# Optimization experiments

Hardware: AMD Instinct MI355X
Metric: run time of the kernel (lower is better)

Reference implementation:

```python
import jax, jax.numpy as jnp
import numpy as np

NUM_HEADS = 4
NUM_GROUPS = 8
EPS = 1e-5


def group_norm(x, gamma, beta):
    # x: [b, c, h, w], GroupNorm with NUM_GROUPS groups, eps=1e-5
    b, c, h, w = x.shape
    xg = x.reshape(b, NUM_GROUPS, (c // NUM_GROUPS) * h * w)
    mean = jnp.mean(xg, axis=-1, keepdims=True)
    var = jnp.var(xg, axis=-1, keepdims=True)
    xn = ((xg - mean) * jax.lax.rsqrt(var + EPS)).reshape(b, c, h, w)
    return xn * gamma[None, :, None, None] + beta[None, :, None, None]


def setup_inputs() -> dict:
    key = jax.random.key(0)
    ks = jax.random.split(key, 4)
    b, c, h, w = 4, 256, 64, 64
    x = jax.random.normal(ks[0], (b, c, h, w), dtype=jnp.float32)
    gamma = jnp.ones((c,), dtype=jnp.float32)
    beta = jnp.zeros((c,), dtype=jnp.float32)
    w_qkv = jax.random.normal(ks[1], (3 * c, c), dtype=jnp.float32) * (c ** -0.5)
    b_qkv = jnp.zeros((3 * c,), dtype=jnp.float32)
    w_proj = jax.random.normal(ks[2], (c, c), dtype=jnp.float32) * (c ** -0.5)
    b_proj = jnp.zeros((c,), dtype=jnp.float32)
    return {"x": x, "gamma": gamma, "beta": beta, "w_qkv": w_qkv,
            "b_qkv": b_qkv, "w_proj": w_proj, "b_proj": b_proj}


def reference(x, gamma, beta, w_qkv, b_qkv, w_proj, b_proj):
    b, c, h, w = x.shape
    heads = NUM_HEADS
    dim = c // heads
    n = h * w
    residual = x
    xn = group_norm(x, gamma, beta)
    # 1x1 conv == per-pixel linear: [b,c,h,w] x [3c,c] -> [b,3c,h,w]
    qkv = jnp.einsum('bchw,oc->bohw', xn, w_qkv) + b_qkv[None, :, None, None]
    # channel layout: (three, heads, dim)
    qkv = qkv.reshape(b, 3, heads, dim, n)            # [b,3,H,D,N]
    qkv = jnp.transpose(qkv, (1, 0, 2, 4, 3))         # [3,b,H,N,D]
    q, k, v = qkv[0], qkv[1], qkv[2]
    scale = dim ** -0.5
    scores = jnp.einsum('bhid,bhjd->bhij', q * scale, k)  # [b,H,N,N]
    attn = jax.nn.softmax(scores, axis=-1)
    out = jnp.einsum('bhij,bhjd->bhid', attn, v)          # [b,H,N,D]
    out = jnp.transpose(out, (0, 1, 3, 2)).reshape(b, c, h, w)
    out = jnp.einsum('bchw,oc->bohw', out, w_proj) + b_proj[None, :, None, None]
    return out + residual
```

## Files before the change

### kernel.cpp

```cpp
#include <hip/hip_runtime.h>
#include <stdint.h>

typedef unsigned short ushort_t;
typedef __attribute__((ext_vector_type(8))) short bf16x8;
typedef __attribute__((ext_vector_type(4))) float f32x4;
typedef __attribute__((ext_vector_type(16))) float f32x16;
typedef __attribute__((ext_vector_type(4))) unsigned int u32x4;

__device__ __forceinline__ ushort_t f2bf(float f) {
  union { float f; unsigned u; } v; v.f = f;
  unsigned r = v.u + 0x7fffu + ((v.u >> 16) & 1u);
  return (ushort_t)(r >> 16);
}
__device__ __forceinline__ unsigned bfbits(float f) {
  union { float f; unsigned u; } v; v.f = f; return v.u;
}
__device__ __forceinline__ unsigned pack_trunc(float lo, float hi) {
#if __has_builtin(__builtin_amdgcn_perm)
  return __builtin_amdgcn_perm(bfbits(hi), bfbits(lo), 0x07060302u);
#else
  return (bfbits(lo) >> 16) | (bfbits(hi) & 0xffff0000u);
#endif
}
__device__ __forceinline__ unsigned pack_rn(float lo, float hi) {
  return (unsigned)f2bf(lo) | ((unsigned)f2bf(hi) << 16);
}
__device__ __forceinline__ void swap32(unsigned &a, unsigned &b) {
#if __has_builtin(__builtin_amdgcn_permlane32_swap)
  auto r = __builtin_amdgcn_permlane32_swap(a, b, false, false);
  a = r[0]; b = r[1];
#else
  asm volatile("v_permlane32_swap_b32 %0, %1" : "+v"(a), "+v"(b));
#endif
}

#define SCALE_Q 0.18033688011112042f
#define EXP_BIAS 23.083109273961734f

__global__ __launch_bounds__(256)
void gn_stats1(const float* __restrict__ x, float2* __restrict__ partial) {
  int blk = blockIdx.x, tid = threadIdx.x;
  const float* base = x + (size_t)blk * 16384;
  float s = 0.f, ss = 0.f;
  for (int i = tid * 4; i < 16384; i += 1024) {
    float4 v = *(const float4*)(base + i);
    s  += v.x + v.y + v.z + v.w;
    ss += v.x*v.x + v.y*v.y + v.z*v.z + v.w*v.w;
  }
  __shared__ float rs[256], rss[256];
  rs[tid] = s; rss[tid] = ss;
  __syncthreads();
  for (int off = 128; off > 0; off >>= 1) {
    if (tid < off) { rs[tid] += rs[tid+off]; rss[tid] += rss[tid+off]; }
    __syncthreads();
  }
  if (tid == 0) partial[blk] = make_float2(rs[0], rss[0]);
}

__global__ __launch_bounds__(64)
void gn_stats2(const float2* __restrict__ partial, float* __restrict__ stats) {
  int g = threadIdx.x;
  if (g < 32) {
    float s = 0.f, ss = 0.f;
    #pragma unroll
    for (int k = 0; k < 8; k++) { float2 p = partial[g*8 + k]; s += p.x; ss += p.y; }
    float mean = s * (1.f/131072.f);
    float var  = ss * (1.f/131072.f) - mean*mean;
    stats[g*2]   = mean;
    stats[g*2+1] = rsqrtf(var + 1e-5f);
  }
}

__global__ __launch_bounds__(256)
void gn_apply_t(const float* __restrict__ x, const float* __restrict__ stats,
                const float* __restrict__ gamma, const float* __restrict__ beta,
                ushort_t* __restrict__ xn_t, int b0) {
  int blk = blockIdx.x;
  int tid = threadIdx.x;
  int ct = blk & 7;
  int nt = (blk >> 3) & 15;
  int bl = blk >> 7;
  int b  = b0 + bl;
  int c0 = ct * 32;
  float mean = stats[(b*8 + ct)*2];
  float rstd = stats[(b*8 + ct)*2 + 1];
  __shared__ ushort_t Ls[32][264];
  for (int idx = tid; idx < 32*64; idx += 256) {
    int cc = idx >> 6, seg = idx & 63;
    float ga = gamma[c0+cc], be = beta[c0+cc];
    float a = rstd * ga;
    float bb = be - mean * a;
    float4 v = *(const float4*)(x + ((size_t)(b*256 + c0 + cc))*4096 + nt*256 + seg*4);
    ushort4 t4 = make_ushort4(f2bf(v.x*a+bb), f2bf(v.y*a+bb), f2bf(v.z*a+bb), f2bf(v.w*a+bb));
    *(ushort4*)&Ls[cc][seg*4] = t4;
  }
  __syncthreads();
  for (int idx = tid; idx < 256*4; idx += 256) {
    int n = idx >> 2, seg = idx & 3;
    union { ushort_t u[8]; uint4 v; } pk;
    #pragma unroll
    for (int e = 0; e < 8; e++) pk.u[e] = Ls[seg*8 + e][n];
    *(uint4*)(xn_t + ((size_t)(bl*4096 + nt*256 + n))*256 + c0 + seg*8) = pk.v;
  }
}

__global__ __launch_bounds__(256)
void wconv2(const float* __restrict__ wq, const float* __restrict__ wp,
            ushort_t* __restrict__ oq, ushort_t* __restrict__ op) {
  int blk = blockIdx.x;
  const float* w; ushort_t* o; int i;
  if (blk < 192) { w = wq; o = oq; i = blk*256 + threadIdx.x; }
  else           { w = wp; o = op; i = (blk-192)*256 + threadIdx.x; }
  float4 v = *(const float4*)(w + (size_t)i*4);
  *(ushort4*)(o + (size_t)i*4) = make_ushort4(f2bf(v.x), f2bf(v.y), f2bf(v.z), f2bf(v.w));
}

__global__ __launch_bounds__(256)
void gemm_qkv(const ushort_t* __restrict__ A, const ushort_t* __restrict__ Bt,
              const float* __restrict__ bias, ushort_t* __restrict__ q,
              ushort_t* __restrict__ kbuf, ushort_t* __restrict__ vt, int b0) {
  int blk = blockIdx.x;
  int nt = blk % 12, mt = blk / 12;
  int m0 = mt*128, n0 = nt*64;
  int tid = threadIdx.x;
  int wave = tid >> 6, lane = tid & 63, quad = lane >> 4, l16 = lane & 15;
  __shared__ ushort_t As[128][40];
  __shared__ ushort_t Bs[64][40];
  __shared__ ushort_t Lt[64][136];
  f32x4 acc[2][4];
  #pragma unroll
  for (int i = 0; i < 2; i++)
    #pragma unroll
    for (int j = 0; j < 4; j++) acc[i][j] = (f32x4){0.f,0.f,0.f,0.f};

  for (int k0 = 0; k0 < 256; k0 += 32) {
    #pragma unroll
    for (int i = tid; i < 512; i += 256) {
      int row = i >> 2, seg = i & 3;
      *(uint4*)&As[row][seg*8] = *(const uint4*)(A + (size_t)(m0+row)*256 + k0 + seg*8);
    }
    {
      int row = tid >> 2, seg = tid & 3;
      *(uint4*)&Bs[row][seg*8] = *(const uint4*)(Bt + (size_t)(n0+row)*256 + k0 + seg*8);
    }
    __syncthreads();
    bf16x8 af[2], bfr[4];
    #pragma unroll
    for (int t = 0; t < 2; t++) af[t]  = *(const bf16x8*)&As[wave*32 + t*16 + l16][quad*8];
    #pragma unroll
    for (int t = 0; t < 4; t++) bfr[t] = *(const bf16x8*)&Bs[t*16 + l16][quad*8];
    #pragma unroll
    for (int ti = 0; ti < 2; ti++)
      #pragma unroll
      for (int jn = 0; jn < 4; jn++)
        acc[ti][jn] = __builtin_amdgcn_mfma_f32_16x16x32_bf16(af[ti], bfr[jn], acc[ti][jn], 0, 0, 0);
    __syncthreads();
  }

  int region = nt >> 2;
  if (region == 0) {
    #pragma unroll
    for (int jn = 0; jn < 4; jn++) {
      int n = n0 + jn*16 + l16;
      float bv = bias[n];
      #pragma unroll
      for (int ti = 0; ti < 2; ti++) {
        int mrow = m0 + wave*32 + ti*16 + quad*4;
        #pragma unroll
        for (int r = 0; r < 4; r++)
          q[(size_t)(b0*4096 + mrow + r)*256 + n] = f2bf((acc[ti][jn][r] + bv) * SCALE_Q);
      }
    }
  } else if (region == 1) {
    #pragma unroll
    for (int jn = 0; jn < 4; jn++) {
      int n = n0 + jn*16 + l16;
      float bv = bias[n];
      #pragma unroll
      for (int ti = 0; ti < 2; ti++) {
        int mrow = m0 + wave*32 + ti*16 + quad*4;
        #pragma unroll
        for (int r = 0; r < 4; r++)
          kbuf[(size_t)(b0*4096 + mrow + r)*256 + (n - 256)] = f2bf(acc[ti][jn][r] + bv);
      }
    }
  } else {
    int hh = nt - 8;
    int b_loc = m0 >> 12;
    #pragma unroll
    for (int jn = 0; jn < 4; jn++) {
      int n = n0 + jn*16 + l16;
      float bv = bias[n];
      int drow = jn*16 + l16;
      #pragma unroll
      for (int ti = 0; ti < 2; ti++) {
        int tcol = wave*32 + ti*16 + quad*4;
        uint2 w;
        w.x = pack_rn(acc[ti][jn][0] + bv, acc[ti][jn][1] + bv);
        w.y = pack_rn(acc[ti][jn][2] + bv, acc[ti][jn][3] + bv);
        *(uint2*)&Lt[drow][tcol] = w;
      }
    }
    __syncthreads();
    size_t vb_ = ((size_t)((b0 + b_loc)*4 + hh)*64)*4096 + (size_t)(m0 & 4095);
    for (int idx = tid; idx < 1024; idx += 256) {
      int dd = idx >> 4, toff = (idx & 15)*8;
      *(uint4*)(vt + vb_ + (size_t)dd*4096 + toff) = *(const uint4*)&Lt[dd][toff];
    }
  }
}

__global__ __launch_bounds__(256, 2)
void attn(ushort_t* __restrict__ q, const ushort_t* __restrict__ k,
          const ushort_t* __restrict__ vt) {
  int blk = blockIdx.x;
  int it = blk & 31;
  int h  = (blk >> 5) & 3;
  int b  = blk >> 7;
  int i0 = it * 128;
  int tid = threadIdx.x;
  int wave = tid >> 6, lane = tid & 63;
  int q32 = lane & 31, hi = lane >> 5;

  __shared__ ushort_t Ks[2][64][72];
  __shared__ ushort_t Vs[2][64][72];

  const ushort_t* kbase = k + (size_t)(b*4096)*256 + h*64;
  const ushort_t* vbase = vt + (size_t)(b*4 + h)*64*4096;
  ushort_t* qrow = q + (size_t)(b*4096 + i0 + wave*32 + q32)*256 + h*64;

  bf16x8 qb0 = *(const bf16x8*)(qrow      + hi*8);
  bf16x8 qb1 = *(const bf16x8*)(qrow + 16 + hi*8);
  bf16x8 qb2 = *(const bf16x8*)(qrow + 32 + hi*8);
  bf16x8 qb3 = *(const bf16x8*)(qrow + 48 + hi*8);

  bf16x8 ones;
  #pragma unroll
  for (int e = 0; e < 8; e++) ones[e] = (short)0x3F80;

  f32x16 bias_init;
  #pragma unroll
  for (int r = 0; r < 16; r++) bias_init[r] = -EXP_BIAS;

  f32x16 o_acc0, o_acc1, l_acc;
  #pragma unroll
  for (int r = 0; r < 16; r++) { o_acc0[r] = 0.f; o_acc1[r] = 0.f; l_acc[r] = 0.f; }

  int sr = tid >> 2, sc = (tid & 3) * 16;
  uint4 rk0, rk1, rv0, rv1;
  #define LOADK(JT) { int j0n = (JT)*64; \
    rk0 = *(const uint4*)(kbase + (size_t)(j0n + sr)*256 + sc); \
    rk1 = *(const uint4*)(kbase + (size_t)(j0n + sr)*256 + sc + 8); }
  #define WRITEK(BI) { \
    *(uint4*)&Ks[BI][sr][sc]     = rk0; \
    *(uint4*)&Ks[BI][sr][sc + 8] = rk1; }
  #define LOADV(JT) { int j0n = (JT)*64; \
    rv0 = *(const uint4*)(vbase + (size_t)sr*4096 + j0n + sc); \
    rv1 = *(const uint4*)(vbase + (size_t)sr*4096 + j0n + sc + 8); }
  #define WRITEV(BI) { \
    *(uint4*)&Vs[BI][sr][sc]     = rv0; \
    *(uint4*)&Vs[BI][sr][sc + 8] = rv1; }

  #define COMPUTE_SUB32(BI, JB) { \
    bf16x8 kb0 = *(const bf16x8*)&Ks[BI][(JB) + q32][hi*8]; \
    bf16x8 kb1 = *(const bf16x8*)&Ks[BI][(JB) + q32][16 + hi*8]; \
    bf16x8 kb2 = *(const bf16x8*)&Ks[BI][(JB) + q32][32 + hi*8]; \
    bf16x8 kb3 = *(const bf16x8*)&Ks[BI][(JB) + q32][48 + hi*8]; \
    __builtin_amdgcn_s_setprio(1); \
    f32x16 s_ = __builtin_amdgcn_mfma_f32_32x32x16_bf16(kb0, qb0, bias_init, 0, 0, 0); \
    s_ = __builtin_amdgcn_mfma_f32_32x32x16_bf16(kb1, qb1, s_, 0, 0, 0); \
    s_ = __builtin_amdgcn_mfma_f32_32x32x16_bf16(kb2, qb2, s_, 0, 0, 0); \
    s_ = __builtin_amdgcn_mfma_f32_32x32x16_bf16(kb3, qb3, s_, 0, 0, 0); \
    _Pragma("unroll") \
    for (int r = 0; r < 16; r++) s_[r] = __builtin_exp2f(s_[r]); \
    unsigned pkA = pack_trunc(s_[0],  s_[1]),  pkB = pack_trunc(s_[2],  s_[3]); \
    unsigned pkC = pack_trunc(s_[4],  s_[5]),  pkD = pack_trunc(s_[6],  s_[7]); \
    unsigned pkE = pack_trunc(s_[8],  s_[9]),  pkF = pack_trunc(s_[10], s_[11]); \
    unsigned pkG = pack_trunc(s_[12], s_[13]), pkH = pack_trunc(s_[14], s_[15]); \
    swap32(pkA, pkC); swap32(pkB, pkD);    \
    swap32(pkE, pkG); swap32(pkF, pkH);    \
    u32x4 w0_ = {pkA, pkB, pkC, pkD}; \
    u32x4 w1_ = {pkE, pkF, pkG, pkH}; \
    bf16x8 pb0 = __builtin_bit_cast(bf16x8, w0_); \
    bf16x8 pb1 = __builtin_bit_cast(bf16x8, w1_); \
    bf16x8 vb00 = *(const bf16x8*)&Vs[BI][q32     ][(JB) + hi*8]; \
    bf16x8 vb01 = *(const bf16x8*)&Vs[BI][q32     ][(JB) + 16 + hi*8]; \
    bf16x8 vb10 = *(const bf16x8*)&Vs[BI][32 + q32][(JB) + hi*8]; \
    bf16x8 vb11 = *(const bf16x8*)&Vs[BI][32 + q32][(JB) + 16 + hi*8]; \
    o_acc0 = __builtin_amdgcn_mfma_f32_32x32x16_bf16(vb00, pb0, o_acc0, 0, 0, 0); \
    o_acc0 = __builtin_amdgcn_mfma_f32_32x32x16_bf16(vb01, pb1, o_acc0, 0, 0, 0); \
    o_acc1 = __builtin_amdgcn_mfma_f32_32x32x16_bf16(vb10, pb0, o_acc1, 0, 0, 0); \
    o_acc1 = __builtin_amdgcn_mfma_f32_32x32x16_bf16(vb11, pb1, o_acc1, 0, 0, 0); \
    l_acc  = __builtin_amdgcn_mfma_f32_32x32x16_bf16(ones, pb0, l_acc, 0, 0, 0); \
    l_acc  = __builtin_amdgcn_mfma_f32_32x32x16_bf16(ones, pb1, l_acc, 0, 0, 0); \
    __builtin_amdgcn_s_setprio(0); \
  }

  LOADK(0); LOADV(0); WRITEK(0); WRITEV(0);
  __syncthreads();

  for (int jt = 0; jt < 64; jt++) {
    int cur = jt & 1;
    if (jt < 63) LOADK(jt + 1);
    COMPUTE_SUB32(cur, 0)
    if (jt < 63) { WRITEK(cur ^ 1); LOADV(jt + 1); }
    COMPUTE_SUB32(cur, 32)
    if (jt < 63) WRITEV(cur ^ 1);
    __syncthreads();
  }
  #undef LOADK
  #undef LOADV
  #undef WRITEK
  #undef WRITEV
  #undef COMPUTE_SUB32

  float inv = 1.f / l_acc[0];

  #pragma unroll
  for (int g = 0; g < 4; g++) {
    ushort4 u;
    u.x = f2bf(o_acc0[g*4+0]*inv); u.y = f2bf(o_acc0[g*4+1]*inv);
    u.z = f2bf(o_acc0[g*4+2]*inv); u.w = f2bf(o_acc0[g*4+3]*inv);
    *(ushort4*)(qrow + g*8 + hi*4) = u;
  }
  #pragma unroll
  for (int g = 0; g < 4; g++) {
    ushort4 u;
    u.x = f2bf(o_acc1[g*4+0]*inv); u.y = f2bf(o_acc1[g*4+1]*inv);
    u.z = f2bf(o_acc1[g*4+2]*inv); u.w = f2bf(o_acc1[g*4+3]*inv);
    *(ushort4*)(qrow + 32 + g*8 + hi*4) = u;
  }
}

__global__ __launch_bounds__(256)
void gemm_proj(const ushort_t* __restrict__ A,
               const ushort_t* __restrict__ Bt,
               const float* __restrict__ bias, const float* __restrict__ resid,
               float* __restrict__ out, int col_base) {
  int blk = blockIdx.x;
  int mt = blk & 1, nt = blk >> 1;
  int m0 = mt*128, n0 = nt*64;
  int tid = threadIdx.x;
  int wave = tid >> 6, lane = tid & 63, quad = lane >> 4, l16 = lane & 15;
  __shared__ ushort_t As[128][40];
  __shared__ ushort_t Bs[64][40];
  f32x4 acc[2][4];
  #pragma unroll
  for (int i = 0; i < 2; i++)
    #pragma unroll
    for (int j = 0; j < 4; j++) acc[i][j] = (f32x4){0.f,0.f,0.f,0.f};

  for (int k0 = 0; k0 < 256; k0 += 32) {
    #pragma unroll
    for (int i = tid; i < 512; i += 256) {
      int row = i >> 2, seg = i & 3;
      *(uint4*)&As[row][seg*8] = *(const uint4*)(A + (size_t)(m0+row)*256 + k0 + seg*8);
    }
    {
      int row = tid >> 2, seg = tid & 3;
      *(uint4*)&Bs[row][seg*8] = *(const uint4*)(Bt + (size_t)(n0+row)*256 + k0 + seg*8);
    }
    __syncthreads();
    bf16x8 af[2], bfr[4];
    #pragma unroll
    for (int t = 0; t < 2; t++) af[t]  = *(const bf16x8*)&As[wave*32 + t*16 + l16][quad*8];
    #pragma unroll
    for (int t = 0; t < 4; t++) bfr[t] = *(const bf16x8*)&Bs[t*16 + l16][quad*8];
    #pragma unroll
    for (int ti = 0; ti < 2; ti++)
      #pragma unroll
      for (int jn = 0; jn < 4; jn++)
        acc[ti][jn] = __builtin_amdgcn_mfma_f32_16x16x32_bf16(af[ti], bfr[jn], acc[ti][jn], 0, 0, 0);
    __syncthreads();
  }
  #pragma unroll
  for (int jn = 0; jn < 4; jn++) {
    int col = col_base + n0 + jn*16 + l16;
    int bb = col >> 12;
    int np = col & 4095;
    #pragma unroll
    for (int ti = 0; ti < 2; ti++) {
      int o = m0 + wave*32 + ti*16 + quad*4;
      #pragma unroll
      for (int r = 0; r < 4; r++) {
        int oo = o + r;
        size_t addr = ((size_t)(bb*256 + oo))*4096 + np;
        out[addr] = acc[ti][jn][r] + bias[oo] + resid[addr];
      }
    }
  }
}

extern "C" void kernel_launch(void* const* d_in, const int* in_sizes, int n_in,
                              void* d_out, int out_size, void* d_ws, size_t ws_size,
                              hipStream_t stream) {
  const float* x      = (const float*)d_in[0];
  const float* gamma  = (const float*)d_in[1];
  const float* beta   = (const float*)d_in[2];
  const float* w_qkv  = (const float*)d_in[3];
  const float* b_qkv  = (const float*)d_in[4];
  const float* w_proj = (const float*)d_in[5];
  const float* b_proj = (const float*)d_in[6];
  float* out = (float*)d_out;

  char* ws = (char*)d_ws;
  float*  stats    = (float*)ws;
  float2* partial  = (float2*)(ws + 1024);
  ushort_t* wqkv_bf  = (ushort_t*)(ws + 4096);
  ushort_t* wproj_bf = (ushort_t*)(ws + 397312);
  char* big = ws + 528384;

  gn_stats1<<<dim3(256), dim3(256), 0, stream>>>(x, partial);
  gn_stats2<<<dim3(1), dim3(64), 0, stream>>>(partial, stats);
  wconv2<<<dim3(256), dim3(256), 0, stream>>>(w_qkv, w_proj, wqkv_bf, wproj_bf);

  if (ws_size >= (size_t)528384 + 3*(size_t)8388608 + (size_t)4194304) {
    ushort_t* q    = (ushort_t*)big;
    ushort_t* kbuf = (ushort_t*)(big + (size_t)8388608);
    ushort_t* vt   = (ushort_t*)(big + (size_t)16777216);
    ushort_t* xn   = (ushort_t*)(big + (size_t)25165824);
    for (int c = 0; c < 2; c++) {
      int b0 = c * 2;
      gn_apply_t<<<dim3(256), dim3(256), 0, stream>>>(x, stats, gamma, beta, xn, b0);
      gemm_qkv<<<dim3(768), dim3(256), 0, stream>>>(xn, wqkv_bf, b_qkv, q, kbuf, vt, b0);
    }
    attn<<<dim3(512), dim3(256), 0, stream>>>(q, kbuf, vt);
    gemm_proj<<<dim3(512), dim3(256), 0, stream>>>(wproj_bf, q, b_proj, x, out, 0);
  } else {
    ushort_t* q_c  = (ushort_t*)big;
    ushort_t* k_c  = (ushort_t*)(big + (size_t)2097152);
    ushort_t* vt_c = (ushort_t*)(big + (size_t)4194304);
    ushort_t* xn_c = (ushort_t*)(big + (size_t)6291456);
    for (int b0 = 0; b0 < 4; b0++) {
      gn_apply_t<<<dim3(128), dim3(256), 0, stream>>>(x, stats, gamma, beta, xn_c, b0);
      gemm_qkv<<<dim3(384), dim3(256), 0, stream>>>(xn_c, wqkv_bf, b_qkv, q_c, k_c, vt_c, 0);
      attn<<<dim3(128), dim3(256), 0, stream>>>(q_c, k_c, vt_c);
      gemm_proj<<<dim3(128), dim3(256), 0, stream>>>(wproj_bf, q_c, b_proj, x, out, b0*4096);
    }
  }
}
```

Before: 246.9 us.

## Split attention KV sequence across wave pairs and merge partial outputs in LDS

The attention kernel now gives each block 64 query rows instead of 128. Its four waves form two pairs, and each pair handles half of the key/value sequence (split-K). Partial output and row-sum accumulators are combined through shared memory at the end, and the grid doubles to 1024 blocks. This is meant to raise the number of blocks and improve occupancy and load balance across CUs. The cost is that each block's K/V tiles are reused by fewer query rows, so L2 traffic for K/V rises, and there is an extra LDS reduction and barrier. Summing the partials without rescaling is valid because the exp uses a fixed bias rather than a running max.

```diff
diff --git a/kernel.cpp b/kernel.cpp
--- a/kernel.cpp
+++ b/kernel.cpp
@@ -214,20 +214,22 @@
 void attn(ushort_t* __restrict__ q, const ushort_t* __restrict__ k,
           const ushort_t* __restrict__ vt) {
   int blk = blockIdx.x;
-  int it = blk & 31;
-  int h  = (blk >> 5) & 3;
-  int b  = blk >> 7;
-  int i0 = it * 128;
+  int it = blk & 63;
+  int h  = (blk >> 6) & 3;
+  int b  = blk >> 8;
+  int i0 = it * 64;
   int tid = threadIdx.x;
   int wave = tid >> 6, lane = tid & 63;
   int q32 = lane & 31, hi = lane >> 5;
-
-  __shared__ ushort_t Ks[2][64][72];
-  __shared__ ushort_t Vs[2][64][72];
-
-  const ushort_t* kbase = k + (size_t)(b*4096)*256 + h*64;
-  const ushort_t* vbase = vt + (size_t)(b*4 + h)*64*4096;
-  ushort_t* qrow = q + (size_t)(b*4096 + i0 + wave*32 + q32)*256 + h*64;
+  int ks = wave >> 1;
+  int qw = wave & 1;
+
+  __shared__ ushort_t Ks[2][2][32][68];
+  __shared__ ushort_t Vs[2][2][64][44];
+
+  const ushort_t* kbase = k + (size_t)(b*4096 + ks*2048)*256 + h*64;
+  const ushort_t* vbase = vt + (size_t)(b*4 + h)*64*4096 + ks*2048;
+  ushort_t* qrow = q + (size_t)(b*4096 + i0 + qw*32 + q32)*256 + h*64;
 
   bf16x8 qb0 = *(const bf16x8*)(qrow      + hi*8);
   bf16x8 qb1 = *(const bf16x8*)(qrow + 16 + hi*8);
@@ -246,26 +248,28 @@
   #pragma unroll
   for (int r = 0; r < 16; r++) { o_acc0[r] = 0.f; o_acc1[r] = 0.f; l_acc[r] = 0.f; }
 
-  int sr = tid >> 2, sc = (tid & 3) * 16;
+  int t = tid & 127, st = tid >> 7;
+  int sr = t >> 2, sc = (t & 3) * 16;
+  int vr = t >> 1, vc = (t & 1) * 16;
   uint4 rk0, rk1, rv0, rv1;
-  #define LOADK(JT) { int j0n = (JT)*64; \
-    rk0 = *(const uint4*)(kbase + (size_t)(j0n + sr)*256 + sc); \
-    rk1 = *(const uint4*)(kbase + (size_t)(j0n + sr)*256 + sc + 8); }
+  #define LOADK(JT) { \
+    rk0 = *(const uint4*)(kbase + (size_t)((JT)*32 + sr)*256 + sc); \
+    rk1 = *(const uint4*)(kbase + (size_t)((JT)*32 + sr)*256 + sc + 8); }
   #define WRITEK(BI) { \
-    *(uint4*)&Ks[BI][sr][sc]     = rk0; \
-    *(uint4*)&Ks[BI][sr][sc + 8] = rk1; }
-  #define LOADV(JT) { int j0n = (JT)*64; \
-    rv0 = *(const uint4*)(vbase + (size_t)sr*4096 + j0n + sc); \
-    rv1 = *(const uint4*)(vbase + (size_t)sr*4096 + j0n + sc + 8); }
+    *(uint4*)&Ks[st][BI][sr][sc]     = rk0; \
+    *(uint4*)&Ks[st][BI][sr][sc + 8] = rk1; }
+  #define LOADV(JT) { \
+    rv0 = *(const uint4*)(vbase + (size_t)vr*4096 + (JT)*32 + vc); \
+    rv1 = *(const uint4*)(vbase + (size_t)vr*4096 + (JT)*32 + vc + 8); }
   #define WRITEV(BI) { \
-    *(uint4*)&Vs[BI][sr][sc]     = rv0; \
-    *(uint4*)&Vs[BI][sr][sc + 8] = rv1; }
-
-  #define COMPUTE_SUB32(BI, JB) { \
-    bf16x8 kb0 = *(const bf16x8*)&Ks[BI][(JB) + q32][hi*8]; \
-    bf16x8 kb1 = *(const bf16x8*)&Ks[BI][(JB) + q32][16 + hi*8]; \
-    bf16x8 kb2 = *(const bf16x8*)&Ks[BI][(JB) + q32][32 + hi*8]; \
-    bf16x8 kb3 = *(const bf16x8*)&Ks[BI][(JB) + q32][48 + hi*8]; \
+    *(uint4*)&Vs[st][BI][vr][vc]     = rv0; \
+    *(uint4*)&Vs[st][BI][vr][vc + 8] = rv1; }
+
+  #define COMPUTE_SUB32(BI) { \
+    bf16x8 kb0 = *(const bf16x8*)&Ks[st][BI][q32][hi*8]; \
+    bf16x8 kb1 = *(const bf16x8*)&Ks[st][BI][q32][16 + hi*8]; \
+    bf16x8 kb2 = *(const bf16x8*)&Ks[st][BI][q32][32 + hi*8]; \
+    bf16x8 kb3 = *(const bf16x8*)&Ks[st][BI][q32][48 + hi*8]; \
     __builtin_amdgcn_s_setprio(1); \
     f32x16 s_ = __builtin_amdgcn_mfma_f32_32x32x16_bf16(kb0, qb0, bias_init, 0, 0, 0); \
     s_ = __builtin_amdgcn_mfma_f32_32x32x16_bf16(kb1, qb1, s_, 0, 0, 0); \
@@ -283,10 +287,10 @@
     u32x4 w1_ = {pkE, pkF, pkG, pkH}; \
     bf16x8 pb0 = __builtin_bit_cast(bf16x8, w0_); \
     bf16x8 pb1 = __builtin_bit_cast(bf16x8, w1_); \
-    bf16x8 vb00 = *(const bf16x8*)&Vs[BI][q32     ][(JB) + hi*8]; \
-    bf16x8 vb01 = *(const bf16x8*)&Vs[BI][q32     ][(JB) + 16 + hi*8]; \
-    bf16x8 vb10 = *(const bf16x8*)&Vs[BI][32 + q32][(JB) + hi*8]; \
-    bf16x8 vb11 = *(const bf16x8*)&Vs[BI][32 + q32][(JB) + 16 + hi*8]; \
+    bf16x8 vb00 = *(const bf16x8*)&Vs[st][BI][q32     ][hi*8]; \
+    bf16x8 vb01 = *(const bf16x8*)&Vs[st][BI][q32     ][16 + hi*8]; \
+    bf16x8 vb10 = *(const bf16x8*)&Vs[st][BI][32 + q32][hi*8]; \
+    bf16x8 vb11 = *(const bf16x8*)&Vs[st][BI][32 + q32][16 + hi*8]; \
     o_acc0 = __builtin_amdgcn_mfma_f32_32x32x16_bf16(vb00, pb0, o_acc0, 0, 0, 0); \
     o_acc0 = __builtin_amdgcn_mfma_f32_32x32x16_bf16(vb01, pb1, o_acc0, 0, 0, 0); \
     o_acc1 = __builtin_amdgcn_mfma_f32_32x32x16_bf16(vb10, pb0, o_acc1, 0, 0, 0); \
@@ -301,11 +305,9 @@
 
   for (int jt = 0; jt < 64; jt++) {
     int cur = jt & 1;
-    if (jt < 63) LOADK(jt + 1);
-    COMPUTE_SUB32(cur, 0)
-    if (jt < 63) { WRITEK(cur ^ 1); LOADV(jt + 1); }
-    COMPUTE_SUB32(cur, 32)
-    if (jt < 63) WRITEV(cur ^ 1);
+    if (jt < 63) { LOADK(jt + 1); LOADV(jt + 1); }
+    COMPUTE_SUB32(cur)
+    if (jt < 63) { WRITEK(cur ^ 1); WRITEV(cur ^ 1); }
     __syncthreads();
   }
   #undef LOADK
@@ -314,21 +316,35 @@
   #undef WRITEV
   #undef COMPUTE_SUB32
 
-  float inv = 1.f / l_acc[0];
-
-  #pragma unroll
-  for (int g = 0; g < 4; g++) {
-    ushort4 u;
-    u.x = f2bf(o_acc0[g*4+0]*inv); u.y = f2bf(o_acc0[g*4+1]*inv);
-    u.z = f2bf(o_acc0[g*4+2]*inv); u.w = f2bf(o_acc0[g*4+3]*inv);
-    *(ushort4*)(qrow + g*8 + hi*4) = u;
-  }
-  #pragma unroll
-  for (int g = 0; g < 4; g++) {
-    ushort4 u;
-    u.x = f2bf(o_acc1[g*4+0]*inv); u.y = f2bf(o_acc1[g*4+1]*inv);
-    u.z = f2bf(o_acc1[g*4+2]*inv); u.w = f2bf(o_acc1[g*4+3]*inv);
-    *(ushort4*)(qrow + 32 + g*8 + hi*4) = u;
+  float* cb = (float*)&Ks[0][0][0][0];
+  if (ks == 1) {
+    float* p = cb + (qw*64 + lane)*34;
+    #pragma unroll
+    for (int r = 0; r < 16; r++) { p[r] = o_acc0[r]; p[16+r] = o_acc1[r]; }
+    p[32] = l_acc[0];
+  }
+  __syncthreads();
+  if (ks == 0) {
+    const float* p = cb + (qw*64 + lane)*34;
+    float inv = 1.f / (l_acc[0] + p[32]);
+    #pragma unroll
+    for (int g = 0; g < 4; g++) {
+      ushort4 u;
+      u.x = f2bf((o_acc0[g*4+0] + p[g*4+0])*inv);
+      u.y = f2bf((o_acc0[g*4+1] + p[g*4+1])*inv);
+      u.z = f2bf((o_acc0[g*4+2] + p[g*4+2])*inv);
+      u.w = f2bf((o_acc0[g*4+3] + p[g*4+3])*inv);
+      *(ushort4*)(qrow + g*8 + hi*4) = u;
+    }
+    #pragma unroll
+    for (int g = 0; g < 4; g++) {
+      ushort4 u;
+      u.x = f2bf((o_acc1[g*4+0] + p[16+g*4+0])*inv);
+      u.y = f2bf((o_acc1[g*4+1] + p[16+g*4+1])*inv);
+      u.z = f2bf((o_acc1[g*4+2] + p[16+g*4+2])*inv);
+      u.w = f2bf((o_acc1[g*4+3] + p[16+g*4+3])*inv);
+      *(ushort4*)(qrow + 32 + g*8 + hi*4) = u;
+    }
   }
 }
 
@@ -424,7 +440,7 @@
       gn_apply_t<<<dim3(256), dim3(256), 0, stream>>>(x, stats, gamma, beta, xn, b0);
       gemm_qkv<<<dim3(768), dim3(256), 0, stream>>>(xn, wqkv_bf, b_qkv, q, kbuf, vt, b0);
     }
-    attn<<<dim3(512), dim3(256), 0, stream>>>(q, kbuf, vt);
+    attn<<<dim3(1024), dim3(256), 0, stream>>>(q, kbuf, vt);
     gemm_proj<<<dim3(512), dim3(256), 0, stream>>>(wproj_bf, q, b_proj, x, out, 0);
   } else {
     ushort_t* q_c  = (ushort_t*)big;
@@ -434,7 +450,7 @@
     for (int b0 = 0; b0 < 4; b0++) {
       gn_apply_t<<<dim3(128), dim3(256), 0, stream>>>(x, stats, gamma, beta, xn_c, b0);
       gemm_qkv<<<dim3(384), dim3(256), 0, stream>>>(xn_c, wqkv_bf, b_qkv, q_c, k_c, vt_c, 0);
-      attn<<<dim3(128), dim3(256), 0, stream>>>(q_c, k_c, vt_c);
+      attn<<<dim3(256), dim3(256), 0, stream>>>(q_c, k_c, vt_c);
       gemm_proj<<<dim3(128), dim3(256), 0, stream>>>(wproj_bf, q_c, b_proj, x, out, b0*4096);
     }
   }
```

New measurement: 262.5 us. 1.06x slower.

## Restructure attention inner loop into 64-key windows with XCD-aware block remap

Applied to the files above, without the earlier changes.

Reworks the attention main loop so each iteration issues both 32-key QK^T MFMA chains together before the two softmax/PV stages. Global K/V loads for the next tile are issued together, with pointer-increment addressing and an unroll of 2. Blocks are remapped so consecutive block ids across the 8 XCDs land on neighbouring tiles for better L2 sharing. exp2 now uses the raw hardware instruction, and the occupancy hint of 2 blocks per CU is dropped from launch bounds. The larger live set (two score tiles, eight K fragments) raises register pressure, which may lower occupancy.

```diff
diff --git a/kernel.cpp b/kernel.cpp
--- a/kernel.cpp
+++ b/kernel.cpp
@@ -31,6 +31,13 @@
   a = r[0]; b = r[1];
 #else
   asm volatile("v_permlane32_swap_b32 %0, %1" : "+v"(a), "+v"(b));
+#endif
+}
+__device__ __forceinline__ float fast_exp2(float x) {
+#if __has_builtin(__builtin_amdgcn_exp2f)
+  return __builtin_amdgcn_exp2f(x);
+#else
+  float r; asm("v_exp_f32 %0, %1" : "=v"(r) : "v"(x)); return r;
 #endif
 }
 
@@ -210,10 +217,11 @@
   }
 }
 
-__global__ __launch_bounds__(256, 2)
+__global__ __launch_bounds__(256)
 void attn(ushort_t* __restrict__ q, const ushort_t* __restrict__ k,
-          const ushort_t* __restrict__ vt) {
-  int blk = blockIdx.x;
+          const ushort_t* __restrict__ vt, int cpx) {
+  int L = blockIdx.x;
+  int blk = (L & 7) * cpx + (L >> 3);
   int it = blk & 31;
   int h  = (blk >> 5) & 3;
   int b  = blk >> 7;
@@ -246,73 +254,100 @@
   #pragma unroll
   for (int r = 0; r < 16; r++) { o_acc0[r] = 0.f; o_acc1[r] = 0.f; l_acc[r] = 0.f; }
 
-  int sr = tid >> 2, sc = (tid & 3) * 16;
+  int srow = tid >> 2, scol = (tid & 3) * 16;
+  const ushort_t* kp = kbase + (size_t)srow*256 + scol;
+  const ushort_t* vp = vbase + (size_t)srow*4096 + scol;
   uint4 rk0, rk1, rv0, rv1;
-  #define LOADK(JT) { int j0n = (JT)*64; \
-    rk0 = *(const uint4*)(kbase + (size_t)(j0n + sr)*256 + sc); \
-    rk1 = *(const uint4*)(kbase + (size_t)(j0n + sr)*256 + sc + 8); }
+  #define LOADK() { \
+    rk0 = *(const uint4*)(kp); \
+    rk1 = *(const uint4*)(kp + 8); \
+    kp += 64*256; }
   #define WRITEK(BI) { \
-    *(uint4*)&Ks[BI][sr][sc]     = rk0; \
-    *(uint4*)&Ks[BI][sr][sc + 8] = rk1; }
-  #define LOADV(JT) { int j0n = (JT)*64; \
-    rv0 = *(const uint4*)(vbase + (size_t)sr*4096 + j0n + sc); \
-    rv1 = *(const uint4*)(vbase + (size_t)sr*4096 + j0n + sc + 8); }
+    *(uint4*)&Ks[BI][srow][scol]     = rk0; \
+    *(uint4*)&Ks[BI][srow][scol + 8] = rk1; }
+  #define LOADV() { \
+    rv0 = *(const uint4*)(vp); \
+    rv1 = *(const uint4*)(vp + 8); \
+    vp += 64; }
   #define WRITEV(BI) { \
-    *(uint4*)&Vs[BI][sr][sc]     = rv0; \
-    *(uint4*)&Vs[BI][sr][sc + 8] = rv1; }
-
-  #define COMPUTE_SUB32(BI, JB) { \
-    bf16x8 kb0 = *(const bf16x8*)&Ks[BI][(JB) + q32][hi*8]; \
-    bf16x8 kb1 = *(const bf16x8*)&Ks[BI][(JB) + q32][16 + hi*8]; \
-    bf16x8 kb2 = *(const bf16x8*)&Ks[BI][(JB) + q32][32 + hi*8]; \
-    bf16x8 kb3 = *(const bf16x8*)&Ks[BI][(JB) + q32][48 + hi*8]; \
+    *(uint4*)&Vs[BI][srow][scol]     = rv0; \
+    *(uint4*)&Vs[BI][srow][scol + 8] = rv1; }
+
+  #define SOFTMAX(S, PB0, PB1) \
+    _Pragma("unroll") \
+    for (int r = 0; r < 16; r++) S[r] = fast_exp2(S[r]); \
+    { unsigned pkA = pack_trunc(S[0],  S[1]),  pkB = pack_trunc(S[2],  S[3]); \
+      unsigned pkC = pack_trunc(S[4],  S[5]),  pkD = pack_trunc(S[6],  S[7]); \
+      unsigned pkE = pack_trunc(S[8],  S[9]),  pkF = pack_trunc(S[10], S[11]); \
+      unsigned pkG = pack_trunc(S[12], S[13]), pkH = pack_trunc(S[14], S[15]); \
+      swap32(pkA, pkC); swap32(pkB, pkD); \
+      swap32(pkE, pkG); swap32(pkF, pkH); \
+      u32x4 w0_ = {pkA, pkB, pkC, pkD}; \
+      u32x4 w1_ = {pkE, pkF, pkG, pkH}; \
+      PB0 = __builtin_bit_cast(bf16x8, w0_); \
+      PB1 = __builtin_bit_cast(bf16x8, w1_); }
+
+  #define WINDOW(BI) { \
+    bf16x8 k00 = *(const bf16x8*)&Ks[BI][q32     ][hi*8]; \
+    bf16x8 k01 = *(const bf16x8*)&Ks[BI][q32     ][16 + hi*8]; \
+    bf16x8 k02 = *(const bf16x8*)&Ks[BI][q32     ][32 + hi*8]; \
+    bf16x8 k03 = *(const bf16x8*)&Ks[BI][q32     ][48 + hi*8]; \
+    bf16x8 k10 = *(const bf16x8*)&Ks[BI][32 + q32][hi*8]; \
+    bf16x8 k11 = *(const bf16x8*)&Ks[BI][32 + q32][16 + hi*8]; \
+    bf16x8 k12 = *(const bf16x8*)&Ks[BI][32 + q32][32 + hi*8]; \
+    bf16x8 k13 = *(const bf16x8*)&Ks[BI][32 + q32][48 + hi*8]; \
     __builtin_amdgcn_s_setprio(1); \
-    f32x16 s_ = __builtin_amdgcn_mfma_f32_32x32x16_bf16(kb0, qb0, bias_init, 0, 0, 0); \
-    s_ = __builtin_amdgcn_mfma_f32_32x32x16_bf16(kb1, qb1, s_, 0, 0, 0); \
-    s_ = __builtin_amdgcn_mfma_f32_32x32x16_bf16(kb2, qb2, s_, 0, 0, 0); \
-    s_ = __builtin_amdgcn_mfma_f32_32x32x16_bf16(kb3, qb3, s_, 0, 0, 0); \
-    _Pragma("unroll") \
-    for (int r = 0; r < 16; r++) s_[r] = __builtin_exp2f(s_[r]); \
-    unsigned pkA = pack_trunc(s_[0],  s_[1]),  pkB = pack_trunc(s_[2],  s_[3]); \
-    unsigned pkC = pack_trunc(s_[4],  s_[5]),  pkD = pack_trunc(s_[6],  s_[7]); \
-    unsigned pkE = pack_trunc(s_[8],  s_[9]),  pkF = pack_trunc(s_[10], s_[11]); \
-    unsigned pkG = pack_trunc(s_[12], s_[13]), pkH = pack_trunc(s_[14], s_[15]); \
-    swap32(pkA, pkC); swap32(pkB, pkD);    \
-    swap32(pkE, pkG); swap32(pkF, pkH);    \
-    u32x4 w0_ = {pkA, pkB, pkC, pkD}; \
-    u32x4 w1_ = {pkE, pkF, pkG, pkH}; \
-    bf16x8 pb0 = __builtin_bit_cast(bf16x8, w0_); \
-    bf16x8 pb1 = __builtin_bit_cast(bf16x8, w1_); \
-    bf16x8 vb00 = *(const bf16x8*)&Vs[BI][q32     ][(JB) + hi*8]; \
-    bf16x8 vb01 = *(const bf16x8*)&Vs[BI][q32     ][(JB) + 16 + hi*8]; \
-    bf16x8 vb10 = *(const bf16x8*)&Vs[BI][32 + q32][(JB) + hi*8]; \
-    bf16x8 vb11 = *(const bf16x8*)&Vs[BI][32 + q32][(JB) + 16 + hi*8]; \
-    o_acc0 = __builtin_amdgcn_mfma_f32_32x32x16_bf16(vb00, pb0, o_acc0, 0, 0, 0); \
-    o_acc0 = __builtin_amdgcn_mfma_f32_32x32x16_bf16(vb01, pb1, o_acc0, 0, 0, 0); \
-    o_acc1 = __builtin_amdgcn_mfma_f32_32x32x16_bf16(vb10, pb0, o_acc1, 0, 0, 0); \
-    o_acc1 = __builtin_amdgcn_mfma_f32_32x32x16_bf16(vb11, pb1, o_acc1, 0, 0, 0); \
-    l_acc  = __builtin_amdgcn_mfma_f32_32x32x16_bf16(ones, pb0, l_acc, 0, 0, 0); \
-    l_acc  = __builtin_amdgcn_mfma_f32_32x32x16_bf16(ones, pb1, l_acc, 0, 0, 0); \
+    f32x16 s0 = __builtin_amdgcn_mfma_f32_32x32x16_bf16(k00, qb0, bias_init, 0, 0, 0); \
+    s0 = __builtin_amdgcn_mfma_f32_32x32x16_bf16(k01, qb1, s0, 0, 0, 0); \
+    s0 = __builtin_amdgcn_mfma_f32_32x32x16_bf16(k02, qb2, s0, 0, 0, 0); \
+    s0 = __builtin_amdgcn_mfma_f32_32x32x16_bf16(k03, qb3, s0, 0, 0, 0); \
+    f32x16 s1 = __builtin_amdgcn_mfma_f32_32x32x16_bf16(k10, qb0, bias_init, 0, 0, 0); \
+    s1 = __builtin_amdgcn_mfma_f32_32x32x16_bf16(k11, qb1, s1, 0, 0, 0); \
+    s1 = __builtin_amdgcn_mfma_f32_32x32x16_bf16(k12, qb2, s1, 0, 0, 0); \
+    s1 = __builtin_amdgcn_mfma_f32_32x32x16_bf16(k13, qb3, s1, 0, 0, 0); \
+    bf16x8 pb00, pb01, pb10, pb11; \
+    SOFTMAX(s0, pb00, pb01)    \
+    { bf16x8 vb00 = *(const bf16x8*)&Vs[BI][q32     ][hi*8]; \
+      bf16x8 vb01 = *(const bf16x8*)&Vs[BI][q32     ][16 + hi*8]; \
+      bf16x8 vb10 = *(const bf16x8*)&Vs[BI][32 + q32][hi*8]; \
+      bf16x8 vb11 = *(const bf16x8*)&Vs[BI][32 + q32][16 + hi*8]; \
+      o_acc0 = __builtin_amdgcn_mfma_f32_32x32x16_bf16(vb00, pb00, o_acc0, 0, 0, 0); \
+      o_acc0 = __builtin_amdgcn_mfma_f32_32x32x16_bf16(vb01, pb01, o_acc0, 0, 0, 0); \
+      o_acc1 = __builtin_amdgcn_mfma_f32_32x32x16_bf16(vb10, pb00, o_acc1, 0, 0, 0); \
+      o_acc1 = __builtin_amdgcn_mfma_f32_32x32x16_bf16(vb11, pb01, o_acc1, 0, 0, 0); \
+      l_acc  = __builtin_amdgcn_mfma_f32_32x32x16_bf16(ones, pb00, l_acc, 0, 0, 0); \
+      l_acc  = __builtin_amdgcn_mfma_f32_32x32x16_bf16(ones, pb01, l_acc, 0, 0, 0); } \
+    SOFTMAX(s1, pb10, pb11)    \
+    { bf16x8 vb00 = *(const bf16x8*)&Vs[BI][q32     ][32 + hi*8]; \
+      bf16x8 vb01 = *(const bf16x8*)&Vs[BI][q32     ][48 + hi*8]; \
+      bf16x8 vb10 = *(const bf16x8*)&Vs[BI][32 + q32][32 + hi*8]; \
+      bf16x8 vb11 = *(const bf16x8*)&Vs[BI][32 + q32][48 + hi*8]; \
+      o_acc0 = __builtin_amdgcn_mfma_f32_32x32x16_bf16(vb00, pb10, o_acc0, 0, 0, 0); \
+      o_acc0 = __builtin_amdgcn_mfma_f32_32x32x16_bf16(vb01, pb11, o_acc0, 0, 0, 0); \
+      o_acc1 = __builtin_amdgcn_mfma_f32_32x32x16_bf16(vb10, pb10, o_acc1, 0, 0, 0); \
+      o_acc1 = __builtin_amdgcn_mfma_f32_32x32x16_bf16(vb11, pb11, o_acc1, 0, 0, 0); \
+      l_acc  = __builtin_amdgcn_mfma_f32_32x32x16_bf16(ones, pb10, l_acc, 0, 0, 0); \
+      l_acc  = __builtin_amdgcn_mfma_f32_32x32x16_bf16(ones, pb11, l_acc, 0, 0, 0); } \
     __builtin_amdgcn_s_setprio(0); \
   }
 
-  LOADK(0); LOADV(0); WRITEK(0); WRITEV(0);
+  LOADK(); LOADV(); WRITEK(0); WRITEV(0);
   __syncthreads();
 
-  for (int jt = 0; jt < 64; jt++) {
-    int cur = jt & 1;
-    if (jt < 63) LOADK(jt + 1);
-    COMPUTE_SUB32(cur, 0)
-    if (jt < 63) { WRITEK(cur ^ 1); LOADV(jt + 1); }
-    COMPUTE_SUB32(cur, 32)
-    if (jt < 63) WRITEV(cur ^ 1);
+  #pragma unroll 2
+  for (int w = 0; w < 64; w++) {
+    int cur = w & 1;
+    if (w < 63) { LOADK(); LOADV(); }
+    WINDOW(cur)
+    if (w < 63) { WRITEK(cur ^ 1); WRITEV(cur ^ 1); }
     __syncthreads();
   }
   #undef LOADK
   #undef LOADV
   #undef WRITEK
   #undef WRITEV
-  #undef COMPUTE_SUB32
+  #undef WINDOW
+  #undef SOFTMAX
 
   float inv = 1.f / l_acc[0];
 
@@ -424,7 +459,7 @@
       gn_apply_t<<<dim3(256), dim3(256), 0, stream>>>(x, stats, gamma, beta, xn, b0);
       gemm_qkv<<<dim3(768), dim3(256), 0, stream>>>(xn, wqkv_bf, b_qkv, q, kbuf, vt, b0);
     }
-    attn<<<dim3(512), dim3(256), 0, stream>>>(q, kbuf, vt);
+    attn<<<dim3(512), dim3(256), 0, stream>>>(q, kbuf, vt, 64);
     gemm_proj<<<dim3(512), dim3(256), 0, stream>>>(wproj_bf, q, b_proj, x, out, 0);
   } else {
     ushort_t* q_c  = (ushort_t*)big;
@@ -434,7 +469,7 @@
     for (int b0 = 0; b0 < 4; b0++) {
       gn_apply_t<<<dim3(128), dim3(256), 0, stream>>>(x, stats, gamma, beta, xn_c, b0);
       gemm_qkv<<<dim3(384), dim3(256), 0, stream>>>(xn_c, wqkv_bf, b_qkv, q_c, k_c, vt_c, 0);
-      attn<<<dim3(128), dim3(256), 0, stream>>>(q_c, k_c, vt_c);
+      attn<<<dim3(128), dim3(256), 0, stream>>>(q_c, k_c, vt_c, 16);
       gemm_proj<<<dim3(128), dim3(256), 0, stream>>>(wproj_bf, q_c, b_proj, x, out, b0*4096);
     }
   }
```

Result: faster. 229.9 us (-6.9%).
